# Optimization experiments

Measured on AMD Instinct MI355X. Metric: run time of the kernel, lower is better.

Reference implementation:

```python
import jax, jax.numpy as jnp
import numpy as np

N_TASK, N_WORKER, N_STATION = 20000, 5000, 1000
D, HEADS, LAYERS = 64, 4, 2
EDGE_COUNTS = [50000, 30000, 30000, 40000, 40000]
# (n_src, n_dst) per relation: precedes, assigned_to, has_task, can_do, done_by
EDGE_SPEC = [(N_TASK, N_TASK), (N_TASK, N_STATION), (N_STATION, N_TASK), (N_WORKER, N_TASK), (N_TASK, N_WORKER)]
EDGE_TYPES = [('task', 'task'), ('task', 'station'), ('station', 'task'), ('worker', 'task'), ('task', 'worker')]


def setup_inputs() -> dict:
    key = jax.random.key(0)
    ks = iter(jax.random.split(key, 64))
    inp = {}
    inp['x_task'] = jax.random.normal(next(ks), (N_TASK, 16), jnp.float32)
    inp['x_worker'] = jax.random.normal(next(ks), (N_WORKER, 12), jnp.float32)
    inp['x_station'] = jax.random.normal(next(ks), (N_STATION, 10), jnp.float32)
    for i, (E, (ns, nd)) in enumerate(zip(EDGE_COUNTS, EDGE_SPEC)):
        src = jax.random.randint(next(ks), (E,), 0, ns)
        dst = jax.random.randint(next(ks), (E,), 0, nd)
        inp[f'ei{i}'] = jnp.stack([src, dst]).astype(jnp.int32)
    def lin(k, i, o):
        return jax.random.normal(k, (i, o), jnp.float32) / np.float32(np.sqrt(i))
    # feature embedder params (Linear + LayerNorm affine) per node type
    for name, fd in [('task', 16), ('worker', 12), ('station', 10)]:
        inp[f'W_{name}'] = lin(next(ks), fd, D)
        inp[f'b_{name}'] = jnp.zeros((D,), jnp.float32)
        inp[f'g_{name}'] = jnp.ones((D,), jnp.float32)
        inp[f'beta_{name}'] = jnp.zeros((D,), jnp.float32)
    # stacked GATv2 params: [layers, 5 edge types, ...]
    inp['gat_Wl'] = jax.random.normal(next(ks), (LAYERS, 5, D, HEADS * D), jnp.float32) / np.float32(np.sqrt(D))
    inp['gat_Wr'] = jax.random.normal(next(ks), (LAYERS, 5, D, HEADS * D), jnp.float32) / np.float32(np.sqrt(D))
    inp['gat_att'] = jax.random.normal(next(ks), (LAYERS, 5, HEADS, D), jnp.float32) * np.float32(0.1)
    inp['gat_bias'] = jnp.zeros((LAYERS, 5, D), jnp.float32)
    return inp


def _layer_norm(x, g, b):
    m = x.mean(-1, keepdims=True)
    v = ((x - m) ** 2).mean(-1, keepdims=True)
    return (x - m) * jax.lax.rsqrt(v + 1e-5) * g + b


def _gatv2(x_src, x_dst, ei, Wl, Wr, att, bias):
    # GATv2Conv, concat=False (mean over heads), no self loops
    n_dst = x_dst.shape[0]
    xl = (x_src @ Wl).reshape(-1, HEADS, D)  # [Ns,H,Dh]
    xr = (x_dst @ Wr).reshape(-1, HEADS, D)  # [Nd,H,Dh]
    src, dst = ei[0], ei[1]
    e = jax.nn.leaky_relu(xl[src] + xr[dst], 0.2)          # [E,H,Dh]
    logits = jnp.einsum('ehd,hd->eh', e, att)              # [E,H]
    m = jax.ops.segment_max(logits, dst, num_segments=n_dst)
    ex = jnp.exp(logits - m[dst])
    denom = jax.ops.segment_sum(ex, dst, num_segments=n_dst)
    alpha = ex / denom[dst]                                # segment softmax per dst node
    out = jax.ops.segment_sum(alpha[..., None] * xl[src], dst, num_segments=n_dst)
    return out.mean(axis=1) + bias                         # [Nd,D]


def _forward(x_task, x_worker, x_station, eis,
             W_task, b_task, g_task, beta_task,
             W_worker, b_worker, g_worker, beta_worker,
             W_station, b_station, g_station, beta_station,
             gat_Wl, gat_Wr, gat_att, gat_bias):
    x = {
        'task': jax.nn.relu(_layer_norm(x_task @ W_task + b_task, g_task, beta_task)),
        'worker': jax.nn.relu(_layer_norm(x_worker @ W_worker + b_worker, g_worker, beta_worker)),
        'station': jax.nn.relu(_layer_norm(x_station @ W_station + b_station, g_station, beta_station)),
    }
    for l in range(LAYERS):
        agg = {'task': 0.0, 'worker': 0.0, 'station': 0.0}
        for t, (st, dt) in enumerate(EDGE_TYPES):
            agg[dt] = agg[dt] + _gatv2(x[st], x[dt], eis[t], gat_Wl[l, t], gat_Wr[l, t], gat_att[l, t], gat_bias[l, t])
        x = {k: jax.nn.relu(agg[k]) + x[k] for k in x}  # HeteroConv sum aggr, then ReLU + residual
    gc = jnp.concatenate([
        x['station'].mean(0), x['task'].mean(0), x['worker'].mean(0),
        x['station'].max(0), x['task'].max(0), x['worker'].max(0),
    ])[None, :]  # [1, 6*D]
    return x['task'], x['worker'], x['station'], gc


def reference(x_task, x_worker, x_station, ei0, ei1, ei2, ei3, ei4,
              W_task, b_task, g_task, beta_task,
              W_worker, b_worker, g_worker, beta_worker,
              W_station, b_station, g_station, beta_station,
              gat_Wl, gat_Wr, gat_att, gat_bias):
    return _forward(x_task, x_worker, x_station, (ei0, ei1, ei2, ei3, ei4),
                    W_task, b_task, g_task, beta_task,
                    W_worker, b_worker, g_worker, beta_worker,
                    W_station, b_station, g_station, beta_station,
                    gat_Wl, gat_Wr, gat_att, gat_bias)
```

## Files before the change

### kernel.cpp

```cpp
#include <hip/hip_runtime.h>
#include <math.h>

#define NT 20000
#define NW 5000
#define NS 1000

typedef __attribute__((ext_vector_type(8))) short bf16x8;
typedef __attribute__((ext_vector_type(4))) float f32x4;

#define CB_T 1250
#define CB_W 313
#define CB_S 63
#define CB_ALL 1626

struct GemmSeg { const short* X; const short* Wt; short* Y; int N; int blk0; };
struct GemmTab { GemmSeg s[10]; int nseg; };

struct GatSeg { const int* rowp; const int* col; const short* xl; const short* xr;
                const float* att; const float* bias; float* agg; int Nd; int wave0; };
struct GatTab { GatSeg s[5]; int nseg; };

struct EdgeSeg { const int* ei; int* cnt; int* col; int E; int blk0; };
struct EdgeTab { EdgeSeg s[5]; int nseg; };

struct ScanTab { int* cnt[5]; int* rowp[5]; int n[5]; };

struct Mega0 {
  const float *xT, *xW, *xS, *WT, *WW, *WS;
  const float *bT, *gT, *beT, *bW, *gW, *beW, *bS, *gS, *beS;
  short *ybT, *ybW, *ybS;
  const float *gWl, *gWr; short *Wlt, *Wrt; int* nxtAll;
};

__device__ __forceinline__ float wsum64(float v) {
  #pragma unroll
  for (int o = 32; o > 0; o >>= 1) v += __shfl_xor(v, o, 64);
  return v;
}
__device__ __forceinline__ short f2b(float f) {
  unsigned u = __float_as_uint(f);
  unsigned r = (u + 0x7FFFu + ((u >> 16) & 1u)) >> 16;
  return (short)(unsigned short)r;
}
__device__ __forceinline__ float blo(unsigned x) { return __uint_as_float(x << 16); }
__device__ __forceinline__ float bhi(unsigned x) { return __uint_as_float(x & 0xFFFF0000u); }

__global__ void mega0_kernel(Mega0 M) {
  int b = blockIdx.x;
  if (b < 6500) {
    int gid = b * 256 + threadIdx.x;
    int wid = gid >> 6, lane = gid & 63;
    const float *x, *W, *bb, *gg, *be; short* yb; int FD, n;
    if (wid < NT)            { x = M.xT; W = M.WT; bb = M.bT; gg = M.gT; be = M.beT; yb = M.ybT; FD = 16; n = wid; }
    else if (wid < NT + NW)  { x = M.xW; W = M.WW; bb = M.bW; gg = M.gW; be = M.beW; yb = M.ybW; FD = 12; n = wid - NT; }
    else                     { x = M.xS; W = M.WS; bb = M.bS; gg = M.gS; be = M.beS; yb = M.ybS; FD = 10; n = wid - NT - NW; }
    const float* xr = x + (size_t)n * FD;
    float acc = bb[lane];
    for (int k = 0; k < FD; ++k) acc = fmaf(xr[k], W[k * 64 + lane], acc);
    float m = wsum64(acc) * (1.f / 64.f);
    float d = acc - m;
    float v = wsum64(d * d) * (1.f / 64.f);
    float o = d * rsqrtf(v + 1e-5f) * gg[lane] + be[lane];
    o = fmaxf(o, 0.f);
    yb[(size_t)n * 64 + lane] = f2b(o);
  } else {
    int idx = (b - 6500) * 256 + threadIdx.x;
    if (idx < 66000) M.nxtAll[idx] = 0;
    int side = idx >= 163840;
    int j = idx - side * 163840;
    int m = j >> 14, e = j & 16383;
    int k = e >> 8, colv = e & 255;
    const float* src = side ? M.gWr : M.gWl;
    short* dst = side ? M.Wrt : M.Wlt;
    dst[m * 16384 + colv * 64 + k] = f2b(src[m * 16384 + e]);
  }
}

__global__ void count_kernel(EdgeTab tab) {
  int b = blockIdx.x, si = 0;
  for (int i = 1; i < tab.nseg; ++i) if (b >= tab.s[i].blk0) si = i;
  EdgeSeg sg = tab.s[si];
  int e = (b - sg.blk0) * 256 + threadIdx.x;
  if (e < sg.E) atomicAdd(&sg.cnt[sg.ei[sg.E + e]], 1);
}

__global__ void scan_kernel(ScanTab tab) {
  int t = blockIdx.x;
  int4* cnt4  = (int4*)tab.cnt[t];
  int*  rowp  = tab.rowp[t];
  int4* rowp4 = (int4*)rowp;
  int n  = tab.n[t];
  int n4 = n >> 2;
  __shared__ int wsums[16];
  __shared__ int carry_s;
  int tid = threadIdx.x, lane = tid & 63, w = tid >> 6;
  if (tid == 0) carry_s = 0;
  __syncthreads();
  for (int base = 0; base < n4; base += 1024) {
    int i = base + tid;
    int4 v = (i < n4) ? cnt4[i] : make_int4(0, 0, 0, 0);
    int tsum = v.x + v.y + v.z + v.w;
    int s = tsum;
    #pragma unroll
    for (int o = 1; o < 64; o <<= 1) { int x = __shfl_up(s, o, 64); if (lane >= o) s += x; }
    if (lane == 63) wsums[w] = s;
    __syncthreads();
    if (w == 0 && lane < 16) {
      int x = wsums[lane];
      #pragma unroll
      for (int o = 1; o < 16; o <<= 1) { int y = __shfl_up(x, o, 16); if (lane >= o) x += y; }
      wsums[lane] = x;
    }
    __syncthreads();
    int carry   = carry_s;
    int waveoff = (w == 0) ? 0 : wsums[w - 1];
    int b0      = carry + waveoff + s - tsum;
    if (i < n4) {
      int4 e;
      e.x = b0; e.y = b0 + v.x; e.z = e.y + v.y; e.w = e.z + v.z;
      rowp4[i] = e;
      cnt4[i]  = e;
    }
    __syncthreads();
    if (tid == 0) carry_s += wsums[15];
    __syncthreads();
  }
  if (threadIdx.x == 0) rowp[n] = carry_s;
}

__global__ void fill_kernel(EdgeTab tab) {
  int b = blockIdx.x, si = 0;
  for (int i = 1; i < tab.nseg; ++i) if (b >= tab.s[i].blk0) si = i;
  EdgeSeg sg = tab.s[si];
  int e = (b - sg.blk0) * 256 + threadIdx.x;
  if (e >= sg.E) return;
  int s = sg.ei[e], d = sg.ei[sg.E + e];
  int pos = atomicAdd(&sg.cnt[d], 1);
  sg.col[pos] = s;
}

__global__ __launch_bounds__(256) void gemm_kernel(GemmTab tab) {
  __shared__ short lds[4096 + 16896];
  int b = blockIdx.x, si = 0;
  for (int i = 1; i < tab.nseg; ++i) if (b >= tab.s[i].blk0) si = i;
  GemmSeg sg = tab.s[si];
  int r0 = (b - sg.blk0) * 64;
  int tid = threadIdx.x;
  #pragma unroll
  for (int it = 0; it < 2; ++it) {
    int idx = it * 256 + tid;
    int row = idx >> 3, kq = idx & 7;
    bf16x8 v = {0, 0, 0, 0, 0, 0, 0, 0};
    if (r0 + row < sg.N) v = *(const bf16x8*)&sg.X[(size_t)(r0 + row) * 64 + kq * 8];
    *(bf16x8*)&lds[(row * 8 + (kq ^ (row & 7))) * 8] = v;
  }
  #pragma unroll
  for (int it = 0; it < 8; ++it) {
    int idx = it * 256 + tid;
    int col = idx >> 3, kq = idx & 7;
    bf16x8 v = *(const bf16x8*)&sg.Wt[col * 64 + kq * 8];
    *(bf16x8*)&lds[4096 + (col * 8 + (kq ^ (col & 7))) * 8] = v;
  }
  __syncthreads();
  int lane = tid & 63, wv = tid >> 6;
  int r = lane & 15, hk = lane >> 4;
  f32x4 acc[4][4];
  #pragma unroll
  for (int rt = 0; rt < 4; ++rt)
    #pragma unroll
    for (int ct = 0; ct < 4; ++ct) acc[rt][ct] = (f32x4){0.f, 0.f, 0.f, 0.f};
  #pragma unroll
  for (int kk = 0; kk < 2; ++kk) {
    int kq = kk * 4 + hk;
    bf16x8 a[4], bb[4];
    #pragma unroll
    for (int rt = 0; rt < 4; ++rt) {
      int row = rt * 16 + r;
      a[rt] = *(const bf16x8*)&lds[(row * 8 + (kq ^ (row & 7))) * 8];
    }
    #pragma unroll
    for (int ct = 0; ct < 4; ++ct) {
      int col = wv * 64 + ct * 16 + r;
      bb[ct] = *(const bf16x8*)&lds[4096 + (col * 8 + (kq ^ (col & 7))) * 8];
    }
    #pragma unroll
    for (int rt = 0; rt < 4; ++rt)
      #pragma unroll
      for (int ct = 0; ct < 4; ++ct)
        acc[rt][ct] = __builtin_amdgcn_mfma_f32_16x16x32_bf16(a[rt], bb[ct], acc[rt][ct], 0, 0, 0);
  }
  __syncthreads();
  #pragma unroll
  for (int rt = 0; rt < 4; ++rt)
    #pragma unroll
    for (int j = 0; j < 4; ++j) {
      int rowl = rt * 16 + hk * 4 + j;
      #pragma unroll
      for (int ct = 0; ct < 4; ++ct)
        lds[rowl * 264 + wv * 64 + ct * 16 + r] = f2b(acc[rt][ct][j]);
    }
  __syncthreads();
  #pragma unroll
  for (int it = 0; it < 8; ++it) {
    int idx = it * 256 + tid;
    int row = idx >> 5, v8 = idx & 31;
    if (r0 + row < sg.N) {
      bf16x8 v = *(const bf16x8*)&lds[row * 264 + v8 * 8];
      *(bf16x8*)&sg.Y[(size_t)(r0 + row) * 256 + v8 * 8] = v;
    }
  }
}

__global__ void gat_kernel(GatTab tab) {
  int gwave = (blockIdx.x * blockDim.x + threadIdx.x) >> 6;
  int lane  = threadIdx.x & 63;
  int si = 0;
  for (int i = 1; i < tab.nseg; ++i) if (gwave >= tab.s[i].wave0) si = i;
  GatSeg sg = tab.s[si];
  int n = gwave - sg.wave0;
  if (n >= sg.Nd) return;
  int h = lane >> 4, lig = lane & 15;
  int beg = sg.rowp[n], end = sg.rowp[n + 1];
  uint2 xru = *(const uint2*)&sg.xr[(size_t)n * 256 + h * 64 + lig * 4];
  float4 a4 = *(const float4*)&sg.att[h * 64 + lig * 4];
  float xr0 = blo(xru.x), xr1 = bhi(xru.x), xr2 = blo(xru.y), xr3 = bhi(xru.y);
  float den = 0.f, c0 = 0.f, c1 = 0.f, c2 = 0.f, c3 = 0.f;
  if (end > beg) {
    int sNxt = sg.col[beg];
    uint2 w = *(const uint2*)&sg.xl[(size_t)sNxt * 256 + h * 64 + lig * 4];
    if (beg + 1 < end) sNxt = sg.col[beg + 1];
    for (int i = beg; i < end; ++i) {
      uint2 wc = w;
      if (i + 1 < end)
        w = *(const uint2*)&sg.xl[(size_t)sNxt * 256 + h * 64 + lig * 4];
      if (i + 2 < end) sNxt = sg.col[i + 2];
      float f0 = blo(wc.x), f1 = bhi(wc.x), f2v = blo(wc.y), f3 = bhi(wc.y);
      float vx = f0 + xr0, vy = f1 + xr1, vz = f2v + xr2, vw = f3 + xr3;
      vx = fmaxf(vx, 0.2f * vx); vy = fmaxf(vy, 0.2f * vy);
      vz = fmaxf(vz, 0.2f * vz); vw = fmaxf(vw, 0.2f * vw);
      float dd = fmaf(vx, a4.x, fmaf(vy, a4.y, fmaf(vz, a4.z, vw * a4.w)));
      dd += __shfl_xor(dd, 1, 64);
      dd += __shfl_xor(dd, 2, 64);
      dd += __shfl_xor(dd, 4, 64);
      dd += __shfl_xor(dd, 8, 64);
      float e = __expf(dd);
      den += e;
      c0 = fmaf(e, f0, c0); c1 = fmaf(e, f1, c1);
      c2 = fmaf(e, f2v, c2); c3 = fmaf(e, f3, c3);
    }
  }
  float o0 = 0.f, o1 = 0.f, o2 = 0.f, o3 = 0.f;
  if (end > beg) {
    float inv = 1.f / den;
    o0 = c0 * inv; o1 = c1 * inv; o2 = c2 * inv; o3 = c3 * inv;
  }
  o0 += __shfl_xor(o0, 16, 64); o0 += __shfl_xor(o0, 32, 64);
  o1 += __shfl_xor(o1, 16, 64); o1 += __shfl_xor(o1, 32, 64);
  o2 += __shfl_xor(o2, 16, 64); o2 += __shfl_xor(o2, 32, 64);
  o3 += __shfl_xor(o3, 16, 64); o3 += __shfl_xor(o3, 32, 64);
  if (lane < 16) {
    float4 b4 = *(const float4*)&sg.bias[lane * 4];
    float4 res;
    res.x = fmaf(0.25f, o0, b4.x); res.y = fmaf(0.25f, o1, b4.y);
    res.z = fmaf(0.25f, o2, b4.z); res.w = fmaf(0.25f, o3, b4.w);
    *(float4*)&sg.agg[(size_t)n * 64 + lane * 4] = res;
  }
}

template <int POOL>
__global__ __launch_bounds__(256) void combine_kernel(
    const float4* __restrict__ aT0, const float4* __restrict__ aT2, const float4* __restrict__ aT3,
    const float4* __restrict__ aW, const float4* __restrict__ aS,
    const uint2* __restrict__ xT, const uint2* __restrict__ xW, const uint2* __restrict__ xS,
    float4* __restrict__ oT, float4* __restrict__ oW, float4* __restrict__ oS,
    uint2* __restrict__ bT, uint2* __restrict__ bW, uint2* __restrict__ bS,
    float4* __restrict__ psum, float4* __restrict__ pmax) {
  int b = blockIdx.x, tid = threadIdx.x;
  const float4 *a; const uint2* x; float4* o; uint2* bo; int n4, local; bool sum3 = false;
  const float4 *a2 = nullptr, *a3 = nullptr;
  if (b < CB_T)              { a = aT0; a2 = aT2; a3 = aT3; x = xT; o = oT; bo = bT; n4 = NT * 16; local = b; sum3 = true; }
  else if (b < CB_T + CB_W)  { a = aW; x = xW; o = oW; bo = bW; n4 = NW * 16; local = b - CB_T; }
  else                       { a = aS; x = xS; o = oS; bo = bS; n4 = NS * 16; local = b - CB_T - CB_W; }
  int j = local * 256 + tid;
  bool valid = j < n4;
  float4 r = make_float4(0.f, 0.f, 0.f, 0.f);
  if (valid) {
    float4 av = a[j];
    if (sum3) {
      float4 v2 = a2[j], v3 = a3[j];
      av.x += v2.x + v3.x; av.y += v2.y + v3.y; av.z += v2.z + v3.z; av.w += v2.w + v3.w;
    }
    uint2 xv = x[j];
    r.x = fmaxf(av.x, 0.f) + blo(xv.x); r.y = fmaxf(av.y, 0.f) + bhi(xv.x);
    r.z = fmaxf(av.z, 0.f) + blo(xv.y); r.w = fmaxf(av.w, 0.f) + bhi(xv.y);
    if (POOL == 0) {
      uint2 pk;
      pk.x = (unsigned)(unsigned short)f2b(r.x) | ((unsigned)(unsigned short)f2b(r.y) << 16);
      pk.y = (unsigned)(unsigned short)f2b(r.z) | ((unsigned)(unsigned short)f2b(r.w) << 16);
      bo[j] = pk;
    } else {
      o[j] = r;
    }
  }
  if (POOL) {
    float4 s = r;
    float4 m = valid ? r : make_float4(-3e38f, -3e38f, -3e38f, -3e38f);
    #pragma unroll
    for (int off = 16; off <= 32; off <<= 1) {
      s.x += __shfl_xor(s.x, off, 64); s.y += __shfl_xor(s.y, off, 64);
      s.z += __shfl_xor(s.z, off, 64); s.w += __shfl_xor(s.w, off, 64);
      m.x = fmaxf(m.x, __shfl_xor(m.x, off, 64)); m.y = fmaxf(m.y, __shfl_xor(m.y, off, 64));
      m.z = fmaxf(m.z, __shfl_xor(m.z, off, 64)); m.w = fmaxf(m.w, __shfl_xor(m.w, off, 64));
    }
    __shared__ float4 ls[4][16], lm[4][16];
    int w = tid >> 6, q = tid & 15;
    if (((tid >> 4) & 3) == 0) { ls[w][q] = s; lm[w][q] = m; }
    __syncthreads();
    if (tid < 16) {
      float4 S = ls[0][tid], M = lm[0][tid];
      #pragma unroll
      for (int i = 1; i < 4; ++i) {
        float4 s2 = ls[i][tid], m2 = lm[i][tid];
        S.x += s2.x; S.y += s2.y; S.z += s2.z; S.w += s2.w;
        M.x = fmaxf(M.x, m2.x); M.y = fmaxf(M.y, m2.y);
        M.z = fmaxf(M.z, m2.z); M.w = fmaxf(M.w, m2.w);
      }
      psum[b * 16 + tid] = S;
      pmax[b * 16 + tid] = M;
    }
  }
}

__global__ void pool2_kernel(const float* __restrict__ psum,
                             const float* __restrict__ pmax,
                             float* __restrict__ gc) {
  int b = blockIdx.x;
  int lane = threadIdx.x & 63, w = threadIdx.x >> 6;
  int off, cnt, N, mi;
  if (b == 0)      { off = CB_T + CB_W; cnt = CB_S; N = NS; mi = 0;   }
  else if (b == 1) { off = 0;           cnt = CB_T; N = NT; mi = 64;  }
  else             { off = CB_T;        cnt = CB_W; N = NW; mi = 128; }
  float s = 0.f, mx = -3e38f;
  for (int i = w; i < cnt; i += 16) {
    s += psum[(size_t)(off + i) * 64 + lane];
    mx = fmaxf(mx, pmax[(size_t)(off + i) * 64 + lane]);
  }
  __shared__ float ss[16][64], sm[16][64];
  ss[w][lane] = s; sm[w][lane] = mx;
  __syncthreads();
  if (w == 0) {
    #pragma unroll
    for (int i = 1; i < 16; ++i) { s += ss[i][lane]; mx = fmaxf(mx, sm[i][lane]); }
    gc[mi + lane] = s / (float)N;
    gc[192 + mi + lane] = mx;
  }
}

extern "C" void kernel_launch(void* const* d_in, const int* in_sizes, int n_in,
                              void* d_out, int out_size, void* d_ws, size_t ws_size,
                              hipStream_t stream) {
  const float* x_in[3] = {(const float*)d_in[0], (const float*)d_in[1], (const float*)d_in[2]};
  const int*   ei[5]   = {(const int*)d_in[3], (const int*)d_in[4], (const int*)d_in[5],
                          (const int*)d_in[6], (const int*)d_in[7]};
  const float* Wemb[3] = {(const float*)d_in[8],  (const float*)d_in[12], (const float*)d_in[16]};
  const float* bemb[3] = {(const float*)d_in[9],  (const float*)d_in[13], (const float*)d_in[17]};
  const float* gemb[3] = {(const float*)d_in[10], (const float*)d_in[14], (const float*)d_in[18]};
  const float* beemb[3]= {(const float*)d_in[11], (const float*)d_in[15], (const float*)d_in[19]};
  const float* gWl   = (const float*)d_in[20];
  const float* gWr   = (const float*)d_in[21];
  const float* gatt  = (const float*)d_in[22];
  const float* gbias = (const float*)d_in[23];

  const int NN[3]  = {NT, NW, NS};
  const int EC[5]  = {50000, 30000, 30000, 40000, 40000};
  const int STy[5] = {0, 0, 2, 1, 0};
  const int DTy[5] = {0, 2, 0, 0, 1};

  char* p = (char*)d_ws;
  auto alloc = [&](size_t bytes) -> void* {
    void* r = (void*)p;
    p += (bytes + 255) & ~(size_t)255;
    return r;
  };
  short* xcb[3];
  for (int k = 0; k < 3; ++k) xcb[k] = (short*)alloc((size_t)NN[k] * 64 * 2);
  float* aggT0 = (float*)alloc((size_t)NT * 64 * 4);
  float* aggT2 = (float*)alloc((size_t)NT * 64 * 4);
  float* aggT3 = (float*)alloc((size_t)NT * 64 * 4);
  float* aggW  = (float*)alloc((size_t)NW * 64 * 4);
  float* aggS  = (float*)alloc((size_t)NS * 64 * 4);
  float* aggOf[5] = {aggT0, aggS, aggT2, aggT3, aggW};
  int* nxtAll = (int*)alloc((size_t)66000 * 4);
  int  nxtOff[5] = {0, NT, NT + NS, 2 * NT + NS, 3 * NT + NS};
  int* nxt[5]; for (int t = 0; t < 5; ++t) nxt[t] = nxtAll + nxtOff[t];
  int *rowp[5], *col[5];
  for (int t = 0; t < 5; ++t) {
    rowp[t] = (int*)alloc((size_t)(NN[DTy[t]] + 1) * 4);
    col[t]  = (int*)alloc((size_t)EC[t] * 4);
  }
  float* psum = (float*)alloc((size_t)CB_ALL * 64 * 4);
  float* pmax = (float*)alloc((size_t)CB_ALL * 64 * 4);
  short* Wlt  = (short*)alloc((size_t)10 * 16384 * 2);
  short* Wrt  = (short*)alloc((size_t)10 * 16384 * 2);
  short *xlT[5], *xrT[5];
  for (int t = 0; t < 5; ++t) {
    xlT[t] = (short*)alloc((size_t)NN[STy[t]] * 256 * 2);
    xrT[t] = (short*)alloc((size_t)NN[DTy[t]] * 256 * 2);
  }

  EdgeTab etab; etab.nseg = 5;
  int eb = 0;
  for (int t = 0; t < 5; ++t) {
    etab.s[t] = {ei[t], nxt[t], col[t], EC[t], eb};
    eb += (EC[t] + 255) / 256;
  }

  Mega0 M;
  M.xT = x_in[0]; M.xW = x_in[1]; M.xS = x_in[2];
  M.WT = Wemb[0]; M.WW = Wemb[1]; M.WS = Wemb[2];
  M.bT = bemb[0]; M.gT = gemb[0]; M.beT = beemb[0];
  M.bW = bemb[1]; M.gW = gemb[1]; M.beW = beemb[1];
  M.bS = bemb[2]; M.gS = gemb[2]; M.beS = beemb[2];
  M.ybT = xcb[0]; M.ybW = xcb[1]; M.ybS = xcb[2];
  M.gWl = gWl; M.gWr = gWr; M.Wlt = Wlt; M.Wrt = Wrt; M.nxtAll = nxtAll;
  mega0_kernel<<<7780, 256, 0, stream>>>(M);

  count_kernel<<<eb, 256, 0, stream>>>(etab);
  ScanTab stab;
  for (int t = 0; t < 5; ++t) { stab.cnt[t] = nxt[t]; stab.rowp[t] = rowp[t]; stab.n[t] = NN[DTy[t]]; }
  scan_kernel<<<5, 1024, 0, stream>>>(stab);
  fill_kernel<<<eb, 256, 0, stream>>>(etab);

  float* outT = (float*)d_out;
  float* outW = outT + (size_t)NT * 64;
  float* outS = outW + (size_t)NW * 64;
  float* gc   = outS + (size_t)NS * 64;

  for (int l = 0; l < 2; ++l) {
    GemmTab gt; gt.nseg = 10;
    int gb = 0;
    for (int t = 0; t < 5; ++t) {
      size_t off = (size_t)(l * 5 + t);
      gt.s[2 * t + 0] = {xcb[STy[t]], Wlt + off * 16384, xlT[t], NN[STy[t]], gb};
      gb += (NN[STy[t]] + 63) / 64;
      gt.s[2 * t + 1] = {xcb[DTy[t]], Wrt + off * 16384, xrT[t], NN[DTy[t]], gb};
      gb += (NN[DTy[t]] + 63) / 64;
    }
    gemm_kernel<<<gb, 256, 0, stream>>>(gt);

    GatTab at; at.nseg = 5;
    const int order[5] = {1, 4, 0, 2, 3};
    int wv = 0;
    for (int oi = 0; oi < 5; ++oi) {
      int t = order[oi];
      size_t off = (size_t)(l * 5 + t);
      at.s[oi] = {rowp[t], col[t], xlT[t], xrT[t], gatt + off * 256, gbias + off * 64,
                  aggOf[t], NN[DTy[t]], wv};
      wv += NN[DTy[t]];
    }
    gat_kernel<<<(wv * 64) / 256, 256, 0, stream>>>(at);

    if (l == 0) {
      combine_kernel<0><<<CB_ALL, 256, 0, stream>>>(
          (const float4*)aggT0, (const float4*)aggT2, (const float4*)aggT3,
          (const float4*)aggW, (const float4*)aggS,
          (const uint2*)xcb[0], (const uint2*)xcb[1], (const uint2*)xcb[2],
          nullptr, nullptr, nullptr,
          (uint2*)xcb[0], (uint2*)xcb[1], (uint2*)xcb[2],
          nullptr, nullptr);
    } else {
      combine_kernel<1><<<CB_ALL, 256, 0, stream>>>(
          (const float4*)aggT0, (const float4*)aggT2, (const float4*)aggT3,
          (const float4*)aggW, (const float4*)aggS,
          (const uint2*)xcb[0], (const uint2*)xcb[1], (const uint2*)xcb[2],
          (float4*)outT, (float4*)outW, (float4*)outS,
          nullptr, nullptr, nullptr,
          (float4*)psum, (float4*)pmax);
    }
  }

  pool2_kernel<<<3, 1024, 0, stream>>>(psum, pmax, gc);
}
```

Baseline: 212.4 us.

## Fuse CSR fill into first GEMM launch and double GEMM row tile

Removes the separate fill_kernel launch and runs its edge-scatter blocks as extra leading blocks of the layer-0 GEMM launch, saving one launch and letting the scatter overlap with the projection GEMMs. The GEMM tile grows from 64 to 128 rows per block so each B tile load is reused across twice as many rows, with output written back in two 64-row halves through LDS. In exchange each thread keeps twice as many accumulators, which raises register pressure and may lower occupancy, and the grid has fewer blocks.

```diff
diff --git a/kernel.cpp b/kernel.cpp
--- a/kernel.cpp
+++ b/kernel.cpp
@@ -128,26 +128,28 @@
   if (threadIdx.x == 0) rowp[n] = carry_s;
 }
 
-__global__ void fill_kernel(EdgeTab tab) {
-  int b = blockIdx.x, si = 0;
-  for (int i = 1; i < tab.nseg; ++i) if (b >= tab.s[i].blk0) si = i;
-  EdgeSeg sg = tab.s[si];
-  int e = (b - sg.blk0) * 256 + threadIdx.x;
-  if (e >= sg.E) return;
-  int s = sg.ei[e], d = sg.ei[sg.E + e];
-  int pos = atomicAdd(&sg.cnt[d], 1);
-  sg.col[pos] = s;
-}
-
-__global__ __launch_bounds__(256) void gemm_kernel(GemmTab tab) {
-  __shared__ short lds[4096 + 16896];
-  int b = blockIdx.x, si = 0;
+__global__ __launch_bounds__(256, 3) void gemm_kernel(GemmTab tab, EdgeTab et, int fillBlocks) {
+  __shared__ short lds[24576];
+  int bx = blockIdx.x;
+  if (bx < fillBlocks) {
+    int si = 0;
+    for (int i = 1; i < et.nseg; ++i) if (bx >= et.s[i].blk0) si = i;
+    EdgeSeg sg = et.s[si];
+    int e = (bx - sg.blk0) * 256 + threadIdx.x;
+    if (e < sg.E) {
+      int s = sg.ei[e], d = sg.ei[sg.E + e];
+      int pos = atomicAdd(&sg.cnt[d], 1);
+      sg.col[pos] = s;
+    }
+    return;
+  }
+  int b = bx - fillBlocks, si = 0;
   for (int i = 1; i < tab.nseg; ++i) if (b >= tab.s[i].blk0) si = i;
   GemmSeg sg = tab.s[si];
-  int r0 = (b - sg.blk0) * 64;
+  int r0 = (b - sg.blk0) * 128;
   int tid = threadIdx.x;
   #pragma unroll
-  for (int it = 0; it < 2; ++it) {
+  for (int it = 0; it < 4; ++it) {
     int idx = it * 256 + tid;
     int row = idx >> 3, kq = idx & 7;
     bf16x8 v = {0, 0, 0, 0, 0, 0, 0, 0};
@@ -159,54 +161,58 @@
     int idx = it * 256 + tid;
     int col = idx >> 3, kq = idx & 7;
     bf16x8 v = *(const bf16x8*)&sg.Wt[col * 64 + kq * 8];
-    *(bf16x8*)&lds[4096 + (col * 8 + (kq ^ (col & 7))) * 8] = v;
+    *(bf16x8*)&lds[8192 + (col * 8 + (kq ^ (col & 7))) * 8] = v;
   }
   __syncthreads();
   int lane = tid & 63, wv = tid >> 6;
   int r = lane & 15, hk = lane >> 4;
-  f32x4 acc[4][4];
-  #pragma unroll
-  for (int rt = 0; rt < 4; ++rt)
+  f32x4 acc[8][4];
+  #pragma unroll
+  for (int rt = 0; rt < 8; ++rt)
     #pragma unroll
     for (int ct = 0; ct < 4; ++ct) acc[rt][ct] = (f32x4){0.f, 0.f, 0.f, 0.f};
   #pragma unroll
   for (int kk = 0; kk < 2; ++kk) {
     int kq = kk * 4 + hk;
-    bf16x8 a[4], bb[4];
-    #pragma unroll
-    for (int rt = 0; rt < 4; ++rt) {
-      int row = rt * 16 + r;
-      a[rt] = *(const bf16x8*)&lds[(row * 8 + (kq ^ (row & 7))) * 8];
-    }
+    bf16x8 bbv[4];
     #pragma unroll
     for (int ct = 0; ct < 4; ++ct) {
       int col = wv * 64 + ct * 16 + r;
-      bb[ct] = *(const bf16x8*)&lds[4096 + (col * 8 + (kq ^ (col & 7))) * 8];
-    }
-    #pragma unroll
-    for (int rt = 0; rt < 4; ++rt)
+      bbv[ct] = *(const bf16x8*)&lds[8192 + (col * 8 + (kq ^ (col & 7))) * 8];
+    }
+    #pragma unroll
+    for (int rt = 0; rt < 8; ++rt) {
+      int row = rt * 16 + r;
+      bf16x8 a = *(const bf16x8*)&lds[(row * 8 + (kq ^ (row & 7))) * 8];
       #pragma unroll
       for (int ct = 0; ct < 4; ++ct)
-        acc[rt][ct] = __builtin_amdgcn_mfma_f32_16x16x32_bf16(a[rt], bb[ct], acc[rt][ct], 0, 0, 0);
-  }
-  __syncthreads();
-  #pragma unroll
-  for (int rt = 0; rt < 4; ++rt)
-    #pragma unroll
-    for (int j = 0; j < 4; ++j) {
-      int rowl = rt * 16 + hk * 4 + j;
+        acc[rt][ct] = __builtin_amdgcn_mfma_f32_16x16x32_bf16(a, bbv[ct], acc[rt][ct], 0, 0, 0);
+    }
+  }
+  #pragma unroll
+  for (int hp = 0; hp < 2; ++hp) {
+    __syncthreads();
+    #pragma unroll
+    for (int rt4 = 0; rt4 < 4; ++rt4) {
+      int rt = hp * 4 + rt4;
       #pragma unroll
-      for (int ct = 0; ct < 4; ++ct)
-        lds[rowl * 264 + wv * 64 + ct * 16 + r] = f2b(acc[rt][ct][j]);
-    }
-  __syncthreads();
-  #pragma unroll
-  for (int it = 0; it < 8; ++it) {
-    int idx = it * 256 + tid;
-    int row = idx >> 5, v8 = idx & 31;
-    if (r0 + row < sg.N) {
-      bf16x8 v = *(const bf16x8*)&lds[row * 264 + v8 * 8];
-      *(bf16x8*)&sg.Y[(size_t)(r0 + row) * 256 + v8 * 8] = v;
+      for (int j = 0; j < 4; ++j) {
+        int rowl = rt4 * 16 + hk * 4 + j;
+        #pragma unroll
+        for (int ct = 0; ct < 4; ++ct)
+          lds[rowl * 264 + wv * 64 + ct * 16 + r] = f2b(acc[rt][ct][j]);
+      }
+    }
+    __syncthreads();
+    #pragma unroll
+    for (int it = 0; it < 8; ++it) {
+      int idx = it * 256 + tid;
+      int rowl = idx >> 5, v8 = idx & 31;
+      int row = hp * 64 + rowl;
+      if (r0 + row < sg.N) {
+        bf16x8 v = *(const bf16x8*)&lds[rowl * 264 + v8 * 8];
+        *(bf16x8*)&sg.Y[(size_t)(r0 + row) * 256 + v8 * 8] = v;
+      }
     }
   }
 }
@@ -429,7 +435,6 @@
   ScanTab stab;
   for (int t = 0; t < 5; ++t) { stab.cnt[t] = nxt[t]; stab.rowp[t] = rowp[t]; stab.n[t] = NN[DTy[t]]; }
   scan_kernel<<<5, 1024, 0, stream>>>(stab);
-  fill_kernel<<<eb, 256, 0, stream>>>(etab);
 
   float* outT = (float*)d_out;
   float* outW = outT + (size_t)NT * 64;
@@ -442,11 +447,12 @@
     for (int t = 0; t < 5; ++t) {
       size_t off = (size_t)(l * 5 + t);
       gt.s[2 * t + 0] = {xcb[STy[t]], Wlt + off * 16384, xlT[t], NN[STy[t]], gb};
-      gb += (NN[STy[t]] + 63) / 64;
+      gb += (NN[STy[t]] + 127) / 128;
       gt.s[2 * t + 1] = {xcb[DTy[t]], Wrt + off * 16384, xrT[t], NN[DTy[t]], gb};
-      gb += (NN[DTy[t]] + 63) / 64;
-    }
-    gemm_kernel<<<gb, 256, 0, stream>>>(gt);
+      gb += (NN[DTy[t]] + 127) / 128;
+    }
+    int fb = (l == 0) ? eb : 0;
+    gemm_kernel<<<fb + gb, 256, 0, stream>>>(gt, etab, fb);
 
     GatTab at; at.nseg = 5;
     const int order[5] = {1, 4, 0, 2, 3};
```

Result: no change. 215.8 us (+1.6%).
